# Kernel tuning notes

Hardware: AMD Instinct MI355X
Metric: run time of the kernel (lower is better)

## Reference

```python
import jax, jax.numpy as jnp
from jax import lax
import numpy as np

IMG = 448          # input image H=W
FEAT = 14          # attention map H=W
STR = IMG // FEAT  # 32: feature->image stride
OUT = 112          # crop resize target
RATIOS = [(4, 4), (3, 5), (5, 3), (6, 6), (5, 7), (7, 5)]
GROUPS = [(0, 3), (3, 6)]   # ratio groups for per-group NMS
N_LIST = [4, 3]
IOU_THRESHS = [0.25, 0.25]
PROPOSALN = 7
CLASSES = 200


def _build_coords():
    coords = []
    for (rh, rw) in RATIOS:
        for r in range(FEAT - rh + 1):
            for c in range(FEAT - rw + 1):
                coords.append([r * STR, c * STR, (r + rh) * STR - 1, (c + rw) * STR - 1])
    return np.array(coords, dtype=np.float32)

COORDS = jnp.asarray(_build_coords())                      # [602, 4] image-space boxes (inclusive)
WINDOW_NUMS = [(FEAT - rh + 1) * (FEAT - rw + 1) for rh, rw in RATIOS]
GROUP_BOUNDS = []
for (s, e) in GROUPS:
    GROUP_BOUNDS.append((sum(WINDOW_NUMS[:s]), sum(WINDOW_NUMS[:e])))


def _window_scores(att):
    # att: [B,1,FEAT,FEAT] -> [B, total_windows]; AvgPool2d(ratio, stride=1) per ratio, flattened row-major
    scs = []
    for (rh, rw) in RATIOS:
        s = lax.reduce_window(att[:, 0], 0.0, lax.add, (1, rh, rw), (1, 1, 1), 'VALID') / (rh * rw)
        scs.append(s.reshape(att.shape[0], -1))
    return jnp.concatenate(scs, axis=1)


def _iou(box, boxes):
    x0 = jnp.maximum(box[0], boxes[:, 0]); y0 = jnp.maximum(box[1], boxes[:, 1])
    x1 = jnp.minimum(box[2], boxes[:, 2]); y1 = jnp.minimum(box[3], boxes[:, 3])
    inter = jnp.maximum(x1 - x0 + 1, 0.0) * jnp.maximum(y1 - y0 + 1, 0.0)
    a1 = (box[2] - box[0] + 1) * (box[3] - box[1] + 1)
    a2 = (boxes[:, 2] - boxes[:, 0] + 1) * (boxes[:, 3] - boxes[:, 1] + 1)
    return inter / (a1 + a2 - inter)


def _nms(scores, boxes, n, thresh):
    # greedy NMS: pick argmax, suppress IoU>thresh, repeat n times
    def step(sc, _):
        idx = jnp.argmax(sc)
        iou = _iou(boxes[idx], boxes)
        sc = jnp.where(iou > thresh, -jnp.inf, sc).at[idx].set(-jnp.inf)
        return sc, idx
    _, idxs = lax.scan(step, scores, None, length=n)
    return idxs.astype(jnp.int32)


def _appm(att):
    all_scores = _window_scores(att)                        # [B, W]
    sg = lax.stop_gradient(all_scores)
    idx_parts = []
    for gi, (gs, ge) in enumerate(GROUP_BOUNDS):
        bx = COORDS[gs:ge]
        f = lambda s: _nms(s, bx, N_LIST[gi], IOU_THRESHS[gi])
        idx_parts.append(jax.vmap(f)(sg[:, gs:ge]) + gs)
    indices = jnp.concatenate(idx_parts, axis=1)            # [B, PROPOSALN]
    win_scores = jnp.take_along_axis(all_scores, indices, axis=1)
    return indices, win_scores, all_scores


_T = jnp.linspace(0.0, 1.0, OUT)


def _crop_resize(img, box):
    # bilinear crop+resize with align_corners=True semantics; img [3,H,W], box [4]
    rs = box[0] + (box[2] - box[0]) * _T
    cs = box[1] + (box[3] - box[1]) * _T
    r0f = jnp.floor(rs); c0f = jnp.floor(cs)
    wr = (rs - r0f)[None, :, None]
    wc = (cs - c0f)[None, None, :]
    r0 = r0f.astype(jnp.int32); c0 = c0f.astype(jnp.int32)
    r1 = jnp.minimum(r0 + 1, IMG - 1); c1 = jnp.minimum(c0 + 1, IMG - 1)
    g = lambda ri, ci: img[:, ri[:, None], ci[None, :]]
    top = (1 - wc) * g(r0, c0) + wc * g(r0, c1)
    bot = (1 - wc) * g(r1, c0) + wc * g(r1, c1)
    return (1 - wr) * top + wr * bot                        # [3, OUT, OUT]


def _encoder(x, ws, bs):
    h = x
    for w, b in zip(ws, bs):
        h = lax.conv_general_dilated(h, w, (2, 2), 'SAME', dimension_numbers=('NCHW', 'OIHW', 'NCHW'))
        h = jax.nn.relu(h + b[None, :, None, None])
    return h


def _head(feat, head_w, head_b):
    return jnp.mean(feat, axis=(2, 3)) @ head_w + head_b


def reference(x, att, w0, b0, w1, b1, w2, b2, w3, b3, w4, b4, head_w, head_b):
    ws = [w0, w1, w2, w3, w4]; bs = [b0, b1, b2, b3, b4]
    B = x.shape[0]
    labels = _head(_encoder(x, ws, bs), head_w, head_b)     # [B, CLASSES]
    indices, win_scores, all_scores = _appm(att)
    boxes = COORDS[indices]                                  # [B, PROPOSALN, 4]
    crop = lambda im, bxs: jax.vmap(lambda b: _crop_resize(im, b))(bxs)
    window_imgs = jax.vmap(crop)(x, boxes)                   # [B, P, 3, OUT, OUT]
    window_imgs = lax.stop_gradient(window_imgs).reshape(B * PROPOSALN, 3, OUT, OUT)  # .detach()
    win_logits = _head(_encoder(window_imgs, ws, bs), head_w, head_b)  # [B*P, CLASSES]
    coordinates = boxes.astype(jnp.int32)
    return labels, win_scores, win_logits, indices, all_scores, coordinates


def setup_inputs() -> dict:
    key = jax.random.key(0)
    ks = jax.random.split(key, 16)
    B = 16
    s = 0.05
    return {
        'x': jax.random.normal(ks[0], (B, 3, IMG, IMG), jnp.float32),
        'att': jax.random.uniform(ks[1], (B, 1, FEAT, FEAT), jnp.float32),
        'w0': jax.random.normal(ks[2], (64, 3, 3, 3), jnp.float32) * s,
        'b0': jax.random.normal(ks[3], (64,), jnp.float32) * s,
        'w1': jax.random.normal(ks[4], (128, 64, 3, 3), jnp.float32) * s,
        'b1': jax.random.normal(ks[5], (128,), jnp.float32) * s,
        'w2': jax.random.normal(ks[6], (256, 128, 3, 3), jnp.float32) * s,
        'b2': jax.random.normal(ks[7], (256,), jnp.float32) * s,
        'w3': jax.random.normal(ks[8], (512, 256, 3, 3), jnp.float32) * s,
        'b3': jax.random.normal(ks[9], (512,), jnp.float32) * s,
        'w4': jax.random.normal(ks[10], (512, 512, 3, 3), jnp.float32) * s,
        'b4': jax.random.normal(ks[11], (512,), jnp.float32) * s,
        'head_w': jax.random.normal(ks[12], (512, CLASSES), jnp.float32) * s,
        'head_b': jax.random.normal(ks[13], (CLASSES,), jnp.float32) * s,
    }
```

## Files before the change

kernel.cpp:

```cpp
#include <hip/hip_runtime.h>
#include <hip/hip_bf16.h>
#include <math.h>


#define OFF_LAB 0
#define OFF_WSC 3200
#define OFF_LOG 3312
#define OFF_IDX 25712
#define OFF_ALL 25824
#define OFF_CRD 35456

#define BS 256

typedef __attribute__((ext_vector_type(8))) short short8;
typedef __attribute__((ext_vector_type(4))) float f32x4;

static inline int cdiv(int a, int b) { return (a + b - 1) / b; }

__device__ __forceinline__ void win_decode(int w, int& rh, int& rw, int& r, int& c) {
  const int RH[6] = {4, 3, 5, 6, 5, 7};
  const int RW[6] = {4, 5, 3, 6, 7, 5};
  int rem = w;
#pragma unroll
  for (int i = 0; i < 6; ++i) {
    int nc = 15 - RW[i];
    int cnt = (15 - RH[i]) * nc;
    if (rem < cnt) { rh = RH[i]; rw = RW[i]; r = rem / nc; c = rem - (rem / nc) * nc; return; }
    rem -= cnt;
  }
  rh = 4; rw = 4; r = 0; c = 0;
}

__device__ __forceinline__ void win_to_box(int w, float* bb) {
  int rh, rw, r, c;
  win_decode(w, rh, rw, r, c);
  bb[0] = r * 32.f;
  bb[1] = c * 32.f;
  bb[2] = (r + rh) * 32.f - 1.f;
  bb[3] = (c + rw) * 32.f - 1.f;
}

__global__ void winscores_kernel(const float* __restrict__ att, float* __restrict__ s_all,
                                 float* __restrict__ out) {
  int idx = blockIdx.x * blockDim.x + threadIdx.x;
  if (idx >= 16 * 602) return;
  int b = idx / 602, w = idx - b * 602;
  int rh, rw, r, c;
  win_decode(w, rh, rw, r, c);
  const float* a = att + b * 196;
  float s = 0.f;
  for (int dr = 0; dr < rh; ++dr)
    for (int dc = 0; dc < rw; ++dc)
      s += a[(r + dr) * 14 + (c + dc)];
  float v = s / (float)(rh * rw);
  s_all[idx] = v;
  out[OFF_ALL + idx] = v;
}

__global__ void nms_kernel(const float* __restrict__ s_all, int* __restrict__ idx_i) {
  const int b = blockIdx.x, g = blockIdx.y;
  const int gs = g ? 361 : 0;
  const int cnt = g ? 241 : 361;
  const int nsel = g ? 3 : 4;
  const int obase = b * 7 + (g ? 4 : 0);
  __shared__ float sc[361];
  __shared__ float bx0[361], bx1[361], bx2[361], bx3[361];
  const int tid = threadIdx.x;
  for (int k = tid; k < cnt; k += 64) {
    sc[k] = s_all[b * 602 + gs + k];
    float bb[4];
    win_to_box(gs + k, bb);
    bx0[k] = bb[0]; bx1[k] = bb[1]; bx2[k] = bb[2]; bx3[k] = bb[3];
  }
  __syncthreads();
  for (int it = 0; it < nsel; ++it) {
    float bv = -INFINITY;
    int bi = 0x7fffffff;
    for (int k = tid; k < cnt; k += 64) {
      float v = sc[k];
      if (v > bv || (v == bv && k < bi)) { bv = v; bi = k; }
    }
#pragma unroll
    for (int off = 32; off > 0; off >>= 1) {
      float ov = __shfl_down(bv, off);
      int oi = __shfl_down(bi, off);
      if (ov > bv || (ov == bv && oi < bi)) { bv = ov; bi = oi; }
    }
    bi = __shfl(bi, 0);
    if (tid == 0) idx_i[obase + it] = gs + bi;
    float X0 = bx0[bi], X1 = bx1[bi], X2 = bx2[bi], X3 = bx3[bi];
    float a1 = (X2 - X0 + 1.f) * (X3 - X1 + 1.f);
    __syncthreads();
    for (int k = tid; k < cnt; k += 64) {
      float x0 = fmaxf(X0, bx0[k]);
      float y0 = fmaxf(X1, bx1[k]);
      float x1 = fminf(X2, bx2[k]);
      float y1 = fminf(X3, bx3[k]);
      float inter = fmaxf(x1 - x0 + 1.f, 0.f) * fmaxf(y1 - y0 + 1.f, 0.f);
      float a2 = (bx2[k] - bx0[k] + 1.f) * (bx3[k] - bx1[k] + 1.f);
      float iou = inter / (a1 + a2 - inter);
      if (iou > 0.25f) sc[k] = -INFINITY;
    }
    if (tid == 0) sc[bi] = -INFINITY;
    __syncthreads();
  }
}

__global__ void gather_kernel(const int* __restrict__ idx_i, const float* __restrict__ s_all,
                              float* __restrict__ boxes, float* __restrict__ out) {
  int t = blockIdx.x * blockDim.x + threadIdx.x;
  if (t >= 112) return;
  int b = t / 7;
  int w = idx_i[t];
  out[OFF_IDX + t] = (float)w;
  out[OFF_WSC + t] = s_all[b * 602 + w];
  float bb[4];
  win_to_box(w, bb);
#pragma unroll
  for (int k = 0; k < 4; ++k) {
    boxes[t * 4 + k] = bb[k];
    out[OFF_CRD + t * 4 + k] = bb[k];
  }
}

__global__ void crop_resize_kernel(const float* __restrict__ x, const float* __restrict__ boxes,
                                   float* __restrict__ wimgs) {
  int idx = blockIdx.x * blockDim.x + threadIdx.x;
  const int total = 112 * 3 * 112 * 112;
  if (idx >= total) return;
  int j = idx % 112;
  int i = (idx / 112) % 112;
  int ch = (idx / (112 * 112)) % 3;
  int bp = idx / (3 * 112 * 112);
  int b = bp / 7;
  const float* bx = boxes + bp * 4;
  float t_i = (float)i / 111.0f;
  float t_j = (float)j / 111.0f;
  float rs = bx[0] + (bx[2] - bx[0]) * t_i;
  float cs = bx[1] + (bx[3] - bx[1]) * t_j;
  float r0f = floorf(rs), c0f = floorf(cs);
  float wr = rs - r0f, wc = cs - c0f;
  int r0 = (int)r0f, c0 = (int)c0f;
  int r1 = min(r0 + 1, 447), c1 = min(c0 + 1, 447);
  const float* img = x + ((size_t)b * 3 + ch) * 448 * 448;
  float v00 = img[r0 * 448 + c0], v01 = img[r0 * 448 + c1];
  float v10 = img[r1 * 448 + c0], v11 = img[r1 * 448 + c1];
  float top = (1.f - wc) * v00 + wc * v01;
  float bot = (1.f - wc) * v10 + wc * v11;
  wimgs[idx] = (1.f - wr) * top + wr * bot;
}

__global__ void zf8_kernel(uint4* __restrict__ p, int n16) {
  int idx = blockIdx.x * blockDim.x + threadIdx.x;
  if (idx < n16) p[idx] = make_uint4(0, 0, 0, 0);
}

__global__ void packw_kernel(const float* __restrict__ w, __hip_bfloat16* __restrict__ dst,
                             int Cout, int Cin) {
  int idx = blockIdx.x * blockDim.x + threadIdx.x;
  int total = Cout * Cin * 9;
  if (idx >= total) return;
  int ci = idx % Cin;
  int rc = idx / Cin;
  int co = rc % Cout;
  int t = rc / Cout;
  dst[idx] = __float2bfloat16(w[((size_t)co * Cin + ci) * 9 + t]);
}

__global__ void packw0_kernel(const float* __restrict__ w, __hip_bfloat16* __restrict__ dst) {
  int idx = blockIdx.x * blockDim.x + threadIdx.x;
  if (idx >= 64 * 32) return;
  int co = idx >> 5, k = idx & 31;
  float v = 0.f;
  if (k < 27) {
    int t = k / 3, c = k - t * 3;
    v = w[((size_t)co * 3 + c) * 9 + t];
  }
  dst[idx] = __float2bfloat16(v);
}

__global__ void im2col3_kernel(const float* __restrict__ x, __hip_bfloat16* __restrict__ A,
                               int N, int Hin, int Hout) {
  int m = blockIdx.x * blockDim.x + threadIdx.x;
  int total = N * Hout * Hout;
  if (m >= total) return;
  int n = m / (Hout * Hout);
  int rem = m - n * (Hout * Hout);
  int oh = rem / Hout, ow = rem - (rem / Hout) * Hout;
  const float* xb = x + (size_t)n * 3 * Hin * Hin;
  __hip_bfloat16* a = A + (size_t)m * 32;
#pragma unroll
  for (int kh = 0; kh < 3; ++kh) {
#pragma unroll
    for (int kw = 0; kw < 3; ++kw) {
      int ih = 2 * oh + kh, iw = 2 * ow + kw;
      bool ok = (ih < Hin) && (iw < Hin);
#pragma unroll
      for (int c = 0; c < 3; ++c) {
        float v = ok ? xb[(size_t)c * Hin * Hin + (size_t)ih * Hin + iw] : 0.f;
        a[(kh * 3 + kw) * 3 + c] = __float2bfloat16(v);
      }
    }
  }
#pragma unroll
  for (int k = 27; k < 32; ++k) a[k] = __float2bfloat16(0.f);
}

template <bool IM2COL>
__global__ __launch_bounds__(512) void conv_mfma_kernel(
    const __hip_bfloat16* __restrict__ in, const __hip_bfloat16* __restrict__ wpk,
    const float* __restrict__ bias, __hip_bfloat16* __restrict__ outp,
    float* __restrict__ pbuf,
    int M, int Hout, int Wout, int Hp, int Wp, int Cin, int Cout, int pad,
    int Hop, int Wop) {
  const int l = threadIdx.x & 63;
  const int w = threadIdx.x >> 6;
  const int px0 = blockIdx.y * 256 + w * 32;
  if (px0 >= M) return;
  const int co0 = blockIdx.x * 64;
  const int half = l >> 4;
  const int lr = l & 15;
  const int HWo = Hout * Wout;

  int mA0 = px0 + lr;      if (mA0 >= M) mA0 = M - 1;
  int mA1 = px0 + 16 + lr; if (mA1 >= M) mA1 = M - 1;
  const __hip_bfloat16* pA0;
  const __hip_bfloat16* pA1;
  if (IM2COL) {
    pA0 = in + (size_t)mA0 * 32 + half * 8;
    pA1 = in + (size_t)mA1 * 32 + half * 8;
  } else {
    int n0 = mA0 / HWo, r0 = mA0 - n0 * HWo, oh0 = r0 / Wout, ow0 = r0 - (r0 / Wout) * Wout;
    int n1 = mA1 / HWo, r1 = mA1 - n1 * HWo, oh1 = r1 / Wout, ow1 = r1 - (r1 / Wout) * Wout;
    pA0 = in + (((size_t)n0 * Hp + (2 * oh0 - pad + 1)) * Wp + (2 * ow0 - pad + 1)) * Cin +
          half * 8;
    pA1 = in + (((size_t)n1 * Hp + (2 * oh1 - pad + 1)) * Wp + (2 * ow1 - pad + 1)) * Cin +
          half * 8;
  }
  const __hip_bfloat16* pB = wpk + (size_t)(co0 + lr) * Cin + half * 8;
  const size_t sCo = (size_t)Cout * Cin;

  f32x4 acc[2][4];
#pragma unroll
  for (int ms = 0; ms < 2; ++ms)
#pragma unroll
    for (int s = 0; s < 4; ++s) acc[ms][s] = (f32x4){0.f, 0.f, 0.f, 0.f};

  const int nq = Cin >> 5;
  const int nqz = nq / gridDim.z;
  const int qlo = blockIdx.z * nqz;
  const int qhi = qlo + nqz;
  for (int q = qlo; q < qhi; ++q) {
    const int q32 = q << 5;
    if (IM2COL) {
      short8 a0 = *(const short8*)(pA0);
      short8 a1 = *(const short8*)(pA1);
#pragma unroll
      for (int s = 0; s < 4; ++s) {
        short8 b = *(const short8*)(pB + (size_t)s * 16 * Cin);
        acc[0][s] = __builtin_amdgcn_mfma_f32_16x16x32_bf16(a0, b, acc[0][s], 0, 0, 0);
        acc[1][s] = __builtin_amdgcn_mfma_f32_16x16x32_bf16(a1, b, acc[1][s], 0, 0, 0);
      }
    } else {
#pragma unroll
      for (int kh = 0; kh < 3; ++kh) {
#pragma unroll
        for (int kw = 0; kw < 3; ++kw) {
          const int dA = (kh * Wp + kw) * Cin + q32;
          short8 a0 = *(const short8*)(pA0 + dA);
          short8 a1 = *(const short8*)(pA1 + dA);
          const __hip_bfloat16* qb = pB + (size_t)(kh * 3 + kw) * sCo + q32;
#pragma unroll
          for (int s = 0; s < 4; ++s) {
            short8 b = *(const short8*)(qb + (size_t)s * 16 * Cin);
            acc[0][s] = __builtin_amdgcn_mfma_f32_16x16x32_bf16(a0, b, acc[0][s], 0, 0, 0);
            acc[1][s] = __builtin_amdgcn_mfma_f32_16x16x32_bf16(a1, b, acc[1][s], 0, 0, 0);
          }
        }
      }
    }
  }

  if (gridDim.z == 1) {
    float bj0 = bias[co0 + lr];
    float bj1 = bias[co0 + 16 + lr];
    float bj2 = bias[co0 + 32 + lr];
    float bj3 = bias[co0 + 48 + lr];
#pragma unroll
    for (int ms = 0; ms < 2; ++ms) {
#pragma unroll
      for (int r = 0; r < 4; ++r) {
        int m = px0 + ms * 16 + half * 4 + r;
        if (m >= M) continue;
        int n = m / HWo, rem = m - n * HWo;
        int oh = rem / Wout, ow = rem - (rem / Wout) * Wout;
        __hip_bfloat16* ob =
            outp + (((size_t)n * Hop + oh + 1) * Wop + (ow + 1)) * Cout + co0 + lr;
        ob[0] = __float2bfloat16(fmaxf(acc[ms][0][r] + bj0, 0.f));
        ob[16] = __float2bfloat16(fmaxf(acc[ms][1][r] + bj1, 0.f));
        ob[32] = __float2bfloat16(fmaxf(acc[ms][2][r] + bj2, 0.f));
        ob[48] = __float2bfloat16(fmaxf(acc[ms][3][r] + bj3, 0.f));
      }
    }
  } else {
    float* pz = pbuf + (size_t)blockIdx.z * M * Cout;
#pragma unroll
    for (int ms = 0; ms < 2; ++ms) {
#pragma unroll
      for (int r = 0; r < 4; ++r) {
        int m = px0 + ms * 16 + half * 4 + r;
        if (m >= M) continue;
        float* pm = pz + (size_t)m * Cout + co0 + lr;
        pm[0] = acc[ms][0][r];
        pm[16] = acc[ms][1][r];
        pm[32] = acc[ms][2][r];
        pm[48] = acc[ms][3][r];
      }
    }
  }
}

__global__ void reduce_nhwc_kernel(const float* __restrict__ pbuf, const float* __restrict__ bias,
                                   __hip_bfloat16* __restrict__ outp, int M, int Cout, int nz,
                                   int Hout, int Wout, int Hop, int Wop) {
  int idx = blockIdx.x * blockDim.x + threadIdx.x;
  if (idx >= M * Cout) return;
  int m = idx / Cout, co = idx - m * Cout;
  float s = 0.f;
  for (int z = 0; z < nz; ++z) s += pbuf[(size_t)z * M * Cout + idx];
  s = fmaxf(s + bias[co], 0.f);
  int HWo = Hout * Wout;
  int n = m / HWo, rem = m - n * HWo;
  int oh = rem / Wout, ow = rem - (rem / Wout) * Wout;
  outp[(((size_t)n * Hop + oh + 1) * Wop + (ow + 1)) * Cout + co] = __float2bfloat16(s);
}

__global__ void avgpool_nhwc_kernel(const __hip_bfloat16* __restrict__ feat,
                                    float* __restrict__ pooled, int Nimg, int H, int Hp, int C) {
  int idx = blockIdx.x * blockDim.x + threadIdx.x;
  if (idx >= Nimg * C) return;
  int n = idx / C, c = idx - n * C;
  float s = 0.f;
  for (int h = 1; h <= H; ++h)
    for (int ww = 1; ww <= H; ++ww)
      s += __bfloat162float(feat[(((size_t)n * Hp + h) * Hp + ww) * C + c]);
  pooled[idx] = s / (float)(H * H);
}

__global__ void head_kernel(const float* __restrict__ pooled, const float* __restrict__ hw,
                            const float* __restrict__ hb, float* __restrict__ outp, int M) {
  int idx = blockIdx.x * blockDim.x + threadIdx.x;
  if (idx >= M * 200) return;
  int m = idx / 200, c = idx - m * 200;
  float acc = hb[c];
  const float* pm = pooled + m * 512;
  for (int k = 0; k < 512; ++k) acc = fmaf(pm[k], hw[k * 200 + c], acc);
  outp[idx] = acc;
}

static void launch_conv(bool im2col, const __hip_bfloat16* in, const __hip_bfloat16* wpk,
                        const float* bv, __hip_bfloat16* dst, float* pbuf, int nz, int M,
                        int Hout, int Hp, int Cin, int Cout, int pad, int Hop, hipStream_t s) {
  dim3 grid(Cout / 64, cdiv(M, 256), nz);
  if (im2col)
    conv_mfma_kernel<true><<<grid, 512, 0, s>>>(in, wpk, bv, dst, pbuf, M, Hout, Hout, Hp, Hp,
                                                Cin, Cout, pad, Hop, Hop);
  else
    conv_mfma_kernel<false><<<grid, 512, 0, s>>>(in, wpk, bv, dst, pbuf, M, Hout, Hout, Hp, Hp,
                                                 Cin, Cout, pad, Hop, Hop);
  if (nz > 1)
    reduce_nhwc_kernel<<<cdiv(M * Cout, BS), BS, 0, s>>>(pbuf, bv, dst, M, Cout, nz, Hout, Hout,
                                                         Hop, Hop);
}

static void zf(__hip_bfloat16* p, size_t n, hipStream_t s) {
  zf8_kernel<<<cdiv((int)(n / 8), BS), BS, 0, s>>>((uint4*)p, (int)(n / 8));
}

extern "C" void kernel_launch(void* const* d_in, const int* in_sizes, int n_in,
                              void* d_out, int out_size, void* d_ws, size_t ws_size,
                              hipStream_t stream) {
  const float* x = (const float*)d_in[0];
  const float* att = (const float*)d_in[1];
  const float* W[5] = {(const float*)d_in[2], (const float*)d_in[4], (const float*)d_in[6],
                       (const float*)d_in[8], (const float*)d_in[10]};
  const float* Bv[5] = {(const float*)d_in[3], (const float*)d_in[5], (const float*)d_in[7],
                        (const float*)d_in[9], (const float*)d_in[11]};
  const float* head_w = (const float*)d_in[12];
  const float* head_b = (const float*)d_in[13];
  float* out = (float*)d_out;
  float* ws = (float*)d_ws;

  size_t o = 0;
  float* s_all = ws + o;  o += 16 * 602;
  int* idx_i = (int*)(ws + o); o += 112;
  float* boxes = ws + o;  o += 112 * 4;
  float* pooled = ws + o; o += (size_t)112 * 512;
  float* wimgs = ws + o;  o += (size_t)112 * 3 * 112 * 112;
  __hip_bfloat16* hb = (__hip_bfloat16*)(ws + o);
  size_t h = 0;
  __hip_bfloat16* wpk0 = hb + h; h += 64 * 32;
  __hip_bfloat16* wpk1 = hb + h; h += (size_t)9 * 128 * 64;
  __hip_bfloat16* wpk2 = hb + h; h += (size_t)9 * 256 * 128;
  __hip_bfloat16* wpk3 = hb + h; h += (size_t)9 * 512 * 256;
  __hip_bfloat16* wpk4 = hb + h; h += (size_t)9 * 512 * 512;
  __hip_bfloat16* A_L0 = hb + h; h += (size_t)200704 * 32;
  __hip_bfloat16* fL3c = A_L0;
  __hip_bfloat16* bufA = hb + h; h += (size_t)4 * 226 * 226 * 64;
  float* pK = (float*)bufA;
  __hip_bfloat16* bufB = hb + h; h += (size_t)4 * 114 * 114 * 128;
  __hip_bfloat16* bufC16 = hb + h; h += (size_t)16 * 58 * 58 * 256;
  __hip_bfloat16* fL3b = hb + h; h += (size_t)16 * 30 * 30 * 512;
  __hip_bfloat16* featB = hb + h; h += (size_t)16 * 16 * 16 * 512;
  __hip_bfloat16* featC = hb + h; h += (size_t)112 * 6 * 6 * 512;

  winscores_kernel<<<cdiv(16 * 602, BS), BS, 0, stream>>>(att, s_all, out);
  nms_kernel<<<dim3(16, 2), 64, 0, stream>>>(s_all, idx_i);
  gather_kernel<<<1, 128, 0, stream>>>(idx_i, s_all, boxes, out);
  crop_resize_kernel<<<cdiv(112 * 3 * 112 * 112, BS), BS, 0, stream>>>(x, boxes, wimgs);

  packw0_kernel<<<cdiv(64 * 32, BS), BS, 0, stream>>>(W[0], wpk0);
  packw_kernel<<<cdiv(9 * 128 * 64, BS), BS, 0, stream>>>(W[1], wpk1, 128, 64);
  packw_kernel<<<cdiv(9 * 256 * 128, BS), BS, 0, stream>>>(W[2], wpk2, 256, 128);
  packw_kernel<<<cdiv(9 * 512 * 256, BS), BS, 0, stream>>>(W[3], wpk3, 512, 256);
  packw_kernel<<<cdiv(9 * 512 * 512, BS), BS, 0, stream>>>(W[4], wpk4, 512, 512);

  zf(bufA, (size_t)4 * 226 * 226 * 64, stream);
  zf(bufB, (size_t)4 * 114 * 114 * 128, stream);
  zf(bufC16, (size_t)16 * 58 * 58 * 256, stream);
  zf(fL3b, (size_t)16 * 30 * 30 * 512, stream);
  zf(featB, (size_t)16 * 16 * 16 * 512, stream);
  for (int chunk = 0; chunk < 4; ++chunk) {
    int n0 = chunk * 4;
    im2col3_kernel<<<cdiv(200704, BS), BS, 0, stream>>>(x + (size_t)n0 * 3 * 448 * 448, A_L0, 4,
                                                        448, 224);
    launch_conv(true, A_L0, wpk0, Bv[0], bufA, nullptr, 1, 200704, 224, 0, 32, 64, 0, 226,
                stream);
    launch_conv(false, bufA, wpk1, Bv[1], bufB, nullptr, 1, 50176, 112, 226, 64, 128, 0, 114,
                stream);
    launch_conv(false, bufB, wpk2, Bv[2], bufC16 + (size_t)n0 * 58 * 58 * 256, nullptr, 1, 12544,
                56, 114, 128, 256, 0, 58, stream);
  }
  launch_conv(false, bufC16, wpk3, Bv[3], fL3b, nullptr, 1, 12544, 28, 58, 256, 512, 0, 30,
              stream);
  launch_conv(false, fL3b, wpk4, Bv[4], featB, pK, 4, 3136, 14, 30, 512, 512, 0, 16, stream);
  avgpool_nhwc_kernel<<<cdiv(16 * 512, BS), BS, 0, stream>>>(featB, pooled, 16, 14, 16, 512);
  head_kernel<<<cdiv(16 * 200, BS), BS, 0, stream>>>(pooled, head_w, head_b, out + OFF_LAB, 16);

  zf(bufA, (size_t)4 * 226 * 226 * 64, stream);
  zf(bufB, (size_t)4 * 114 * 114 * 128, stream);
  zf(bufC16, (size_t)16 * 58 * 58 * 256, stream);
  zf(featC, (size_t)112 * 6 * 6 * 512, stream);
  for (int chunk = 0; chunk < 2; ++chunk) {
    int c0 = chunk * 56;
    im2col3_kernel<<<cdiv(175616, BS), BS, 0, stream>>>(wimgs + (size_t)c0 * 3 * 112 * 112, A_L0,
                                                        56, 112, 56);
    launch_conv(true, A_L0, wpk0, Bv[0], bufA, nullptr, 1, 175616, 56, 0, 32, 64, 0, 58, stream);
    launch_conv(false, bufA, wpk1, Bv[1], bufB, nullptr, 1, 43904, 28, 58, 64, 128, 0, 30,
                stream);
    launch_conv(false, bufB, wpk2, Bv[2], bufC16 + (size_t)c0 * 16 * 16 * 256, nullptr, 1, 10976,
                14, 30, 128, 256, 0, 16, stream);
  }
  zf(fL3c, (size_t)112 * 9 * 9 * 512, stream);
  launch_conv(false, bufC16, wpk3, Bv[3], fL3c, pK, 2, 5488, 7, 16, 256, 512, 0, 9, stream);
  launch_conv(false, fL3c, wpk4, Bv[4], featC, pK, 4, 1792, 4, 9, 512, 512, 1, 6, stream);
  avgpool_nhwc_kernel<<<cdiv(112 * 512, BS), BS, 0, stream>>>(featC, pooled, 112, 4, 6, 512);
  head_kernel<<<cdiv(112 * 200, BS), BS, 0, stream>>>(pooled, head_w, head_b, out + OFF_LOG, 112);
}
```

Baseline: 1.704 ms.

## Use 128x128 block tiles and double-K unroll for non-im2col convs

For the direct (non-im2col) conv path, each 512-thread block now covers 128 pixels by 128 output channels (4x2 wave arrangement) instead of 256 pixels by 64 channels, which changes how A and B fragments are reused across waves through cache. The inner K loop is also unrolled by two 32-channel slices, so more independent loads are issued before the MFMAs. The unroll assumes the per-split channel count is even, and it raises register pressure. A local variable was also renamed.

```diff
diff --git a/kernel.cpp b/kernel.cpp
--- a/kernel.cpp
+++ b/kernel.cpp
@@ -206,7 +206,7 @@
   for (int k = 27; k < 32; ++k) a[k] = __float2bfloat16(0.f);
 }
 
-template <bool IM2COL>
+template <bool IM2COL, bool WIDE>
 __global__ __launch_bounds__(512) void conv_mfma_kernel(
     const __hip_bfloat16* __restrict__ in, const __hip_bfloat16* __restrict__ wpk,
     const float* __restrict__ bias, __hip_bfloat16* __restrict__ outp,
@@ -215,9 +215,15 @@
     int Hop, int Wop) {
   const int l = threadIdx.x & 63;
   const int w = threadIdx.x >> 6;
-  const int px0 = blockIdx.y * 256 + w * 32;
+  int px0, co0;
+  if (WIDE) {
+    px0 = blockIdx.y * 128 + (w & 3) * 32;
+    co0 = blockIdx.x * 128 + (w >> 2) * 64;
+  } else {
+    px0 = blockIdx.y * 256 + w * 32;
+    co0 = blockIdx.x * 64;
+  }
   if (px0 >= M) return;
-  const int co0 = blockIdx.x * 64;
   const int half = l >> 4;
   const int lr = l & 15;
   const int HWo = Hout * Wout;
@@ -250,9 +256,8 @@
   const int nqz = nq / gridDim.z;
   const int qlo = blockIdx.z * nqz;
   const int qhi = qlo + nqz;
-  for (int q = qlo; q < qhi; ++q) {
-    const int q32 = q << 5;
-    if (IM2COL) {
+  if (IM2COL) {
+    for (int q = qlo; q < qhi; ++q) {
       short8 a0 = *(const short8*)(pA0);
       short8 a1 = *(const short8*)(pA1);
 #pragma unroll
@@ -261,20 +266,28 @@
         acc[0][s] = __builtin_amdgcn_mfma_f32_16x16x32_bf16(a0, b, acc[0][s], 0, 0, 0);
         acc[1][s] = __builtin_amdgcn_mfma_f32_16x16x32_bf16(a1, b, acc[1][s], 0, 0, 0);
       }
-    } else {
+    }
+  } else {
+    for (int q = qlo; q < qhi; q += 2) {
+      const int qa = q << 5, qb32 = qa + 32;
 #pragma unroll
       for (int kh = 0; kh < 3; ++kh) {
 #pragma unroll
         for (int kw = 0; kw < 3; ++kw) {
-          const int dA = (kh * Wp + kw) * Cin + q32;
-          short8 a0 = *(const short8*)(pA0 + dA);
-          short8 a1 = *(const short8*)(pA1 + dA);
-          const __hip_bfloat16* qb = pB + (size_t)(kh * 3 + kw) * sCo + q32;
+          const int dA = (kh * Wp + kw) * Cin;
+          short8 a00 = *(const short8*)(pA0 + dA + qa);
+          short8 a01 = *(const short8*)(pA0 + dA + qb32);
+          short8 a10 = *(const short8*)(pA1 + dA + qa);
+          short8 a11 = *(const short8*)(pA1 + dA + qb32);
+          const __hip_bfloat16* qw = pB + (size_t)(kh * 3 + kw) * sCo;
 #pragma unroll
           for (int s = 0; s < 4; ++s) {
-            short8 b = *(const short8*)(qb + (size_t)s * 16 * Cin);
-            acc[0][s] = __builtin_amdgcn_mfma_f32_16x16x32_bf16(a0, b, acc[0][s], 0, 0, 0);
-            acc[1][s] = __builtin_amdgcn_mfma_f32_16x16x32_bf16(a1, b, acc[1][s], 0, 0, 0);
+            short8 b0 = *(const short8*)(qw + (size_t)s * 16 * Cin + qa);
+            short8 b1 = *(const short8*)(qw + (size_t)s * 16 * Cin + qb32);
+            acc[0][s] = __builtin_amdgcn_mfma_f32_16x16x32_bf16(a00, b0, acc[0][s], 0, 0, 0);
+            acc[0][s] = __builtin_amdgcn_mfma_f32_16x16x32_bf16(a01, b1, acc[0][s], 0, 0, 0);
+            acc[1][s] = __builtin_amdgcn_mfma_f32_16x16x32_bf16(a10, b0, acc[1][s], 0, 0, 0);
+            acc[1][s] = __builtin_amdgcn_mfma_f32_16x16x32_bf16(a11, b1, acc[1][s], 0, 0, 0);
           }
         }
       }
@@ -361,13 +374,15 @@
 static void launch_conv(bool im2col, const __hip_bfloat16* in, const __hip_bfloat16* wpk,
                         const float* bv, __hip_bfloat16* dst, float* pbuf, int nz, int M,
                         int Hout, int Hp, int Cin, int Cout, int pad, int Hop, hipStream_t s) {
-  dim3 grid(Cout / 64, cdiv(M, 256), nz);
-  if (im2col)
-    conv_mfma_kernel<true><<<grid, 512, 0, s>>>(in, wpk, bv, dst, pbuf, M, Hout, Hout, Hp, Hp,
-                                                Cin, Cout, pad, Hop, Hop);
-  else
-    conv_mfma_kernel<false><<<grid, 512, 0, s>>>(in, wpk, bv, dst, pbuf, M, Hout, Hout, Hp, Hp,
-                                                 Cin, Cout, pad, Hop, Hop);
+  if (im2col) {
+    dim3 grid(Cout / 64, cdiv(M, 256), nz);
+    conv_mfma_kernel<true, false><<<grid, 512, 0, s>>>(in, wpk, bv, dst, pbuf, M, Hout, Hout, Hp,
+                                                       Hp, Cin, Cout, pad, Hop, Hop);
+  } else {
+    dim3 grid(Cout / 128, cdiv(M, 128), nz);
+    conv_mfma_kernel<false, true><<<grid, 512, 0, s>>>(in, wpk, bv, dst, pbuf, M, Hout, Hout, Hp,
+                                                       Hp, Cin, Cout, pad, Hop, Hop);
+  }
   if (nz > 1)
     reduce_nhwc_kernel<<<cdiv(M * Cout, BS), BS, 0, s>>>(pbuf, bv, dst, M, Cout, nz, Hout, Hout,
                                                          Hop, Hop);
@@ -397,22 +412,22 @@
   float* boxes = ws + o;  o += 112 * 4;
   float* pooled = ws + o; o += (size_t)112 * 512;
   float* wimgs = ws + o;  o += (size_t)112 * 3 * 112 * 112;
-  __hip_bfloat16* hb = (__hip_bfloat16*)(ws + o);
+  __hip_bfloat16* hbb = (__hip_bfloat16*)(ws + o);
   size_t h = 0;
-  __hip_bfloat16* wpk0 = hb + h; h += 64 * 32;
-  __hip_bfloat16* wpk1 = hb + h; h += (size_t)9 * 128 * 64;
-  __hip_bfloat16* wpk2 = hb + h; h += (size_t)9 * 256 * 128;
-  __hip_bfloat16* wpk3 = hb + h; h += (size_t)9 * 512 * 256;
-  __hip_bfloat16* wpk4 = hb + h; h += (size_t)9 * 512 * 512;
-  __hip_bfloat16* A_L0 = hb + h; h += (size_t)200704 * 32;
+  __hip_bfloat16* wpk0 = hbb + h; h += 64 * 32;
+  __hip_bfloat16* wpk1 = hbb + h; h += (size_t)9 * 128 * 64;
+  __hip_bfloat16* wpk2 = hbb + h; h += (size_t)9 * 256 * 128;
+  __hip_bfloat16* wpk3 = hbb + h; h += (size_t)9 * 512 * 256;
+  __hip_bfloat16* wpk4 = hbb + h; h += (size_t)9 * 512 * 512;
+  __hip_bfloat16* A_L0 = hbb + h; h += (size_t)200704 * 32;
   __hip_bfloat16* fL3c = A_L0;
-  __hip_bfloat16* bufA = hb + h; h += (size_t)4 * 226 * 226 * 64;
+  __hip_bfloat16* bufA = hbb + h; h += (size_t)4 * 226 * 226 * 64;
   float* pK = (float*)bufA;
-  __hip_bfloat16* bufB = hb + h; h += (size_t)4 * 114 * 114 * 128;
-  __hip_bfloat16* bufC16 = hb + h; h += (size_t)16 * 58 * 58 * 256;
-  __hip_bfloat16* fL3b = hb + h; h += (size_t)16 * 30 * 30 * 512;
-  __hip_bfloat16* featB = hb + h; h += (size_t)16 * 16 * 16 * 512;
-  __hip_bfloat16* featC = hb + h; h += (size_t)112 * 6 * 6 * 512;
+  __hip_bfloat16* bufB = hbb + h; h += (size_t)4 * 114 * 114 * 128;
+  __hip_bfloat16* bufC16 = hbb + h; h += (size_t)16 * 58 * 58 * 256;
+  __hip_bfloat16* fL3b = hbb + h; h += (size_t)16 * 30 * 30 * 512;
+  __hip_bfloat16* featB = hbb + h; h += (size_t)16 * 16 * 16 * 512;
+  __hip_bfloat16* featC = hbb + h; h += (size_t)112 * 6 * 6 * 512;
 
   winscores_kernel<<<cdiv(16 * 602, BS), BS, 0, stream>>>(att, s_all, out);
   nms_kernel<<<dim3(16, 2), 64, 0, stream>>>(s_all, idx_i);
```

New measurement: 1.712 ms. No clear change (+0.5%).
